# Performance work log

Measured on AMD Instinct MI355X. Metric: run time of the kernel, lower is better.

Reference implementation:

```python
import jax, jax.numpy as jnp
import numpy as np

EXPERT_NUM = 8
SEQ_LEN = 4096
FREQ_LEN = SEQ_LEN // 2 + 1


def setup_inputs() -> dict:
    key = jax.random.key(0)
    ks = jax.random.split(key, 6)
    B, C = 32, 8
    x = jax.random.normal(ks[0], (B, C, SEQ_LEN), dtype=jnp.float32)
    raw = jax.random.uniform(ks[1], (EXPERT_NUM - 1,), dtype=jnp.float32)
    s1 = 1.0 / np.sqrt(FREQ_LEN)
    W1 = jax.random.uniform(ks[2], (FREQ_LEN, FREQ_LEN), jnp.float32, -s1, s1)
    b1 = jax.random.uniform(ks[3], (FREQ_LEN,), jnp.float32, -s1, s1)
    W2 = jax.random.uniform(ks[4], (EXPERT_NUM, FREQ_LEN), jnp.float32, -s1, s1)
    b2 = jax.random.uniform(ks[5], (EXPERT_NUM,), jnp.float32, -s1, s1)
    return {"x": x, "raw": raw, "W1": W1, "b1": b1, "W2": W2, "b2": b2}


def reference(x, raw, W1, b1, W2, b2):
    # instance norm over seq dim (unbiased variance, like torch.var default)
    x_mean = jnp.mean(x, axis=2, keepdims=True)
    xc = x - x_mean
    n = x.shape[2]
    x_var = jnp.sum(xc * xc, axis=2, keepdims=True) / (n - 1) + 1e-5
    xn = xc / jnp.sqrt(x_var)

    freq_x = jnp.fft.rfft(xn, axis=-1)            # [B, C, F] complex
    F_ = freq_x.shape[-1]

    # sorted sigmoid boundaries -> integer band edges (non-differentiable cast)
    b = jnp.sort(jax.nn.sigmoid(raw))
    boundaries = jnp.concatenate([jnp.zeros(1, x.dtype), b, jnp.ones(1, x.dtype)])
    idx = jnp.floor(jax.lax.stop_gradient(boundaries) * F_).astype(jnp.int32)
    idx = idx.at[-1].set(F_)

    # band-pass masks for all experts at once: [E, F]
    fpos = jnp.arange(F_)
    mask = (fpos[None, :] >= idx[:-1, None]) & (fpos[None, :] < idx[1:, None])

    # per-expert frequency components: [B, E, C, F]
    comp = freq_x[:, None, :, :] * mask[None, :, None, :].astype(freq_x.dtype)
    expert_outputs = jnp.fft.irfft(comp, n=SEQ_LEN, axis=-1)  # [B, E, C, L]

    # gating on channel-averaged magnitude spectrum
    gating_input = jnp.mean(jnp.abs(freq_x), axis=1)          # [B, F]
    h = jax.nn.relu(gating_input @ W1.T + b1)
    gating_scores = jax.nn.softmax(h @ W2.T + b2, axis=-1)    # [B, E]

    # gated combine in frequency domain, then single iFFT
    gate_c = gating_scores.astype(freq_x.dtype)
    combined_freq = jnp.einsum('becf,be->bcf', comp, gate_c)
    combined = jnp.fft.irfft(combined_freq, n=SEQ_LEN, axis=-1)
    combined = combined * jnp.sqrt(x_var) + x_mean
    return combined, boundaries, gating_scores, expert_outputs
```

## Files before the change

### kernel.cpp

```cpp
#include <hip/hip_runtime.h>
#include <hip/hip_bf16.h>


using cplx = float2;
typedef float nfloat2 __attribute__((ext_vector_type(2)));

static constexpr int BB = 32, CCH = 8, LL = 4096, FF = 2049, EE = 8;

static constexpr size_t WS_FREQ  = 0;
static constexpr size_t WS_MEAN  = WS_FREQ + (size_t)BB * CCH * FF * 2;
static constexpr size_t WS_SIGMA = WS_MEAN + 256;
static constexpr size_t WS_GI    = WS_SIGMA + 256;
static constexpr size_t WS_H     = WS_GI + (size_t)BB * FF;
static constexpr size_t WS_IDX   = WS_H + (size_t)BB * FF;
static constexpr size_t WS_EOF   = WS_IDX + 16;
static constexpr size_t WS_LOGIT = WS_EOF + 2049;
static constexpr size_t WS_W2048 = WS_LOGIT + 256;
static constexpr size_t WS_U     = WS_W2048 + 4096;

static constexpr size_t OUT_COMB = 0;
static constexpr size_t OUT_BND  = (size_t)BB * CCH * LL;
static constexpr size_t OUT_GATE = OUT_BND + 9;
static constexpr size_t OUT_EXP  = OUT_GATE + (size_t)BB * EE;

#define PHI(i) ((i) + ((i) >> 5))
__device__ __forceinline__ int scat(int n) {
  return ((n & 3) << 9) | (((n >> 2) & 7) << 6) | (((n >> 5) & 7) << 3) | (n >> 8);
}

template <bool INV>
__device__ __forceinline__ void dft8(float* zr, float* zi) {
  const float C = 0.70710678118654752f;
  float s0r = zr[0] + zr[4], s0i = zi[0] + zi[4];
  float d0r = zr[0] - zr[4], d0i = zi[0] - zi[4];
  float s1r = zr[2] + zr[6], s1i = zi[2] + zi[6];
  float d1r = zr[2] - zr[6], d1i = zi[2] - zi[6];
  float E0r = s0r + s1r, E0i = s0i + s1i;
  float E2r = s0r - s1r, E2i = s0i - s1i;
  float E1r, E1i, E3r, E3i;
  if (!INV) { E1r = d0r + d1i; E1i = d0i - d1r; E3r = d0r - d1i; E3i = d0i + d1r; }
  else      { E1r = d0r - d1i; E1i = d0i + d1r; E3r = d0r + d1i; E3i = d0i - d1r; }
  float t0r = zr[1] + zr[5], t0i = zi[1] + zi[5];
  float e0r = zr[1] - zr[5], e0i = zi[1] - zi[5];
  float t1r = zr[3] + zr[7], t1i = zi[3] + zi[7];
  float e1r = zr[3] - zr[7], e1i = zi[3] - zi[7];
  float O0r = t0r + t1r, O0i = t0i + t1i;
  float O2r = t0r - t1r, O2i = t0i - t1i;
  float O1r, O1i, O3r, O3i;
  if (!INV) { O1r = e0r + e1i; O1i = e0i - e1r; O3r = e0r - e1i; O3i = e0i + e1r; }
  else      { O1r = e0r - e1i; O1i = e0i + e1r; O3r = e0r + e1i; O3i = e0i - e1r; }
  float w1r, w1i, w2r, w2i, w3r, w3i;
  if (!INV) {
    w1r = C * (O1r + O1i); w1i = C * (O1i - O1r);
    w2r = O2i;             w2i = -O2r;
    w3r = C * (O3i - O3r); w3i = -C * (O3r + O3i);
  } else {
    w1r = C * (O1r - O1i); w1i = C * (O1i + O1r);
    w2r = -O2i;            w2i = O2r;
    w3r = -C * (O3r + O3i); w3i = C * (O3r - O3i);
  }
  zr[0] = E0r + O0r; zi[0] = E0i + O0i;
  zr[4] = E0r - O0r; zi[4] = E0i - O0i;
  zr[1] = E1r + w1r; zi[1] = E1i + w1i;
  zr[5] = E1r - w1r; zi[5] = E1i - w1i;
  zr[2] = E2r + w2r; zi[2] = E2i + w2i;
  zr[6] = E2r - w2r; zi[6] = E2i - w2i;
  zr[3] = E3r + w3r; zi[3] = E3i + w3i;
  zr[7] = E3r - w3r; zi[7] = E3i - w3i;
}

template <bool INV>
__device__ __forceinline__ void dft4(float* zr, float* zi) {
  float s0r = zr[0] + zr[2], s0i = zi[0] + zi[2];
  float d0r = zr[0] - zr[2], d0i = zi[0] - zi[2];
  float s1r = zr[1] + zr[3], s1i = zi[1] + zi[3];
  float d1r = zr[1] - zr[3], d1i = zi[1] - zi[3];
  zr[0] = s0r + s1r; zi[0] = s0i + s1i;
  zr[2] = s0r - s1r; zi[2] = s0i - s1i;
  if (!INV) { zr[1] = d0r + d1i; zi[1] = d0i - d1r; zr[3] = d0r - d1i; zi[3] = d0i + d1r; }
  else      { zr[1] = d0r - d1i; zi[1] = d0i + d1r; zr[3] = d0r + d1i; zi[3] = d0i - d1r; }
}

template <bool INV>
__device__ void fftr8(float* ZR, float* ZI, const cplx* __restrict__ W, int t) {
  float zr[8], zi[8];
  {
    int base = 8 * t;
#pragma unroll
    for (int m = 0; m < 8; ++m) { int i = PHI(base + m); zr[m] = ZR[i]; zi[m] = ZI[i]; }
    dft8<INV>(zr, zi);
#pragma unroll
    for (int m = 0; m < 8; ++m) { int i = PHI(base + m); ZR[i] = zr[m]; ZI[i] = zi[m]; }
  }
  __syncthreads();
  {
    int g = t & 31, p = t >> 5;
    int base = 64 * g + p;
#pragma unroll
    for (int m = 0; m < 8; ++m) { int i = PHI(base + 8 * m); zr[m] = ZR[i]; zi[m] = ZI[i]; }
#pragma unroll
    for (int m = 1; m < 8; ++m) {
      cplx w = W[32 * m * p];
      float wi = INV ? -w.y : w.y;
      float xr = zr[m] * w.x - zi[m] * wi;
      float xi = zr[m] * wi + zi[m] * w.x;
      zr[m] = xr; zi[m] = xi;
    }
    dft8<INV>(zr, zi);
#pragma unroll
    for (int m = 0; m < 8; ++m) { int i = PHI(base + 8 * m); ZR[i] = zr[m]; ZI[i] = zi[m]; }
  }
  __syncthreads();
  {
    int g = t & 3, p = t >> 2;
    int base = 512 * g + p;
#pragma unroll
    for (int m = 0; m < 8; ++m) { int i = PHI(base + 64 * m); zr[m] = ZR[i]; zi[m] = ZI[i]; }
#pragma unroll
    for (int m = 1; m < 8; ++m) {
      cplx w = W[4 * m * p];
      float wi = INV ? -w.y : w.y;
      float xr = zr[m] * w.x - zi[m] * wi;
      float xi = zr[m] * wi + zi[m] * w.x;
      zr[m] = xr; zi[m] = xi;
    }
    dft8<INV>(zr, zi);
#pragma unroll
    for (int m = 0; m < 8; ++m) { int i = PHI(base + 64 * m); ZR[i] = zr[m]; ZI[i] = zi[m]; }
  }
  __syncthreads();
  {
#pragma unroll
    for (int h = 0; h < 2; ++h) {
      int p = t + (h << 8);
      float yr[4], yi[4];
#pragma unroll
      for (int m = 0; m < 4; ++m) { int i = PHI(p + 512 * m); yr[m] = ZR[i]; yi[m] = ZI[i]; }
#pragma unroll
      for (int m = 1; m < 4; ++m) {
        cplx w = W[m * p];
        float wi = INV ? -w.y : w.y;
        float xr = yr[m] * w.x - yi[m] * wi;
        float xi = yr[m] * wi + yi[m] * w.x;
        yr[m] = xr; yi[m] = xi;
      }
      dft4<INV>(yr, yi);
#pragma unroll
      for (int m = 0; m < 4; ++m) { int i = PHI(p + 512 * m); ZR[i] = yr[m]; ZI[i] = yi[m]; }
    }
  }
  __syncthreads();
}

__global__ void k_misc(const float* __restrict__ raw,
                       float* __restrict__ out,
                       float* __restrict__ ws) {
  const int blk = blockIdx.x, t = threadIdx.x;
  if (blk < 8) {
    int j = blk * 256 + t;
    float sn, cs;
    sincosf(-6.283185307179586f * (float)j / 2048.0f, &sn, &cs);
    ((cplx*)(ws + WS_W2048))[j] = make_float2(cs, sn);
  } else if (blk < 17) {
    int k = (blk - 8) * 256 + t;
    if (k < FF) {
      float sn, cs;
      sincosf(-3.14159265358979323846f * (float)k / 2048.0f, &sn, &cs);
      ((cplx*)(ws + WS_U))[k] = make_float2(cs, sn);
    }
  } else if (blk == 17) {
    __shared__ int idx_s[9];
    if (t == 0) {
      float v[7];
      for (int i = 0; i < 7; ++i) v[i] = 1.0f / (1.0f + expf(-raw[i]));
      for (int a = 1; a < 7; ++a) {
        float key = v[a];
        int q = a - 1;
        while (q >= 0 && v[q] > key) { v[q + 1] = v[q]; --q; }
        v[q + 1] = key;
      }
      float bnd[9];
      bnd[0] = 0.0f; bnd[8] = 1.0f;
      for (int i = 0; i < 7; ++i) bnd[i + 1] = v[i];
      int* wi = (int*)(ws + WS_IDX);
      for (int e = 0; e < 9; ++e) {
        int id = (int)floorf(bnd[e] * (float)FF);
        if (e == 8) id = FF;
        idx_s[e] = id;
        wi[e] = id;
        out[OUT_BND + e] = bnd[e];
      }
    }
    __syncthreads();
    int* eof = (int*)(ws + WS_EOF);
    for (int f = t; f < FF; f += 256) {
      int e = 0;
      for (int q = 1; q < 8; ++q)
        if (f >= idx_s[q]) e = q;
      eof[f] = e;
    }
  } else {
    float4* p = (float4*)(ws + WS_GI);
    const float4 z4 = make_float4(0.f, 0.f, 0.f, 0.f);
    for (int i = (blk - 18) * 256 + t; i < 32784; i += 32 * 256) p[i] = z4;
  }
}

__global__ __launch_bounds__(256) void k_fwd(const float* __restrict__ x,
                                             float* __restrict__ ws) {
  __shared__ float ZR[2112], ZI[2112];
  __shared__ float red[8];
  const int t  = threadIdx.x;
  const int bc = blockIdx.x;
  const int b  = bc >> 3;
  const int lane = t & 63, wid = t >> 6;
  const cplx* W = (const cplx*)(ws + WS_W2048);
  const cplx* U = (const cplx*)(ws + WS_U);
  const float2* xp2 = (const float2*)(x + (size_t)bc * LL);

  float2 v[8];
  float sum = 0.f;
#pragma unroll
  for (int u = 0; u < 8; ++u) {
    v[u] = xp2[t + (u << 8)];
    sum += v[u].x + v[u].y;
  }
#pragma unroll
  for (int off = 32; off > 0; off >>= 1) sum += __shfl_down(sum, off, 64);
  if (lane == 0) red[wid] = sum;
  __syncthreads();
  const float mean = (red[0] + red[1] + red[2] + red[3]) * (1.0f / 4096.0f);

  float ss = 0.f;
#pragma unroll
  for (int u = 0; u < 8; ++u) {
    float dx = v[u].x - mean, dy = v[u].y - mean;
    ss += dx * dx + dy * dy;
  }
#pragma unroll
  for (int off = 32; off > 0; off >>= 1) ss += __shfl_down(ss, off, 64);
  if (lane == 0) red[4 + wid] = ss;
  __syncthreads();
  const float var   = (red[4] + red[5] + red[6] + red[7]) / 4095.0f + 1e-5f;
  const float sigma = sqrtf(var);
  const float inv   = 1.0f / sigma;
  if (t == 0) {
    ws[WS_MEAN + bc]  = mean;
    ws[WS_SIGMA + bc] = sigma;
  }

#pragma unroll
  for (int u = 0; u < 8; ++u) {
    int n = t + (u << 8);
    int i = PHI(scat(n));
    ZR[i] = (v[u].x - mean) * inv;
    ZI[i] = (v[u].y - mean) * inv;
  }
  __syncthreads();

  fftr8<false>(ZR, ZI, W, t);

  cplx* freq = (cplx*)ws + (size_t)bc * FF;
#pragma unroll
  for (int u = 0; u < 9; ++u) {
    int k = t + (u << 8);
    if (k > 2048) break;
    int ka = k & 2047, km = (2048 - k) & 2047;
    float Zkr = ZR[PHI(ka)], Zki = ZI[PHI(ka)];
    float Zmr = ZR[PHI(km)], Zmi = ZI[PHI(km)];
    float fex = 0.5f * (Zkr + Zmr);
    float fey = 0.5f * (Zki - Zmi);
    float fox = 0.5f * (Zki + Zmi);
    float foy = -0.5f * (Zkr - Zmr);
    cplx uk = U[k];
    float rx = fex + uk.x * fox - uk.y * foy;
    float ry = fey + uk.x * foy + uk.y * fox;
    freq[k] = make_float2(rx, ry);
    atomicAdd(&ws[WS_GI + (size_t)b * FF + k], 0.125f * sqrtf(rx * rx + ry * ry));
  }
}

__global__ __launch_bounds__(256) void k_mid(const float* __restrict__ W1,
                                             float* __restrict__ ws,
                                             float* __restrict__ out) {
  __shared__ float SM[4224];
  const int p = blockIdx.x, t = threadIdx.x;

  if (p < 1089) {
    float* W1s = SM;
    float* gis = SM + 2112;
    const int i0 = (p % 33) * 64;
    const int il = t & 63, bg = t >> 6;
    float acc[8] = {0, 0, 0, 0, 0, 0, 0, 0};
    const int fbeg = (p / 33) * 64;
    const int fend = min(fbeg + 64, FF);
    for (int f0 = fbeg; f0 < fend; f0 += 32) {
      for (int q = t; q < 64 * 32; q += 256) {
        int r = q >> 5, cc = q & 31;
        int gi_i = i0 + r, gf = f0 + cc;
        W1s[r * 33 + cc] = (gi_i < FF && gf < FF) ? W1[(size_t)gi_i * FF + gf] : 0.f;
      }
      for (int q = t; q < 32 * 32; q += 256) {
        int bb = q >> 5, cc = q & 31;
        int gf = f0 + cc;
        gis[bb * 33 + cc] = (gf < FF) ? ws[WS_GI + (size_t)bb * FF + gf] : 0.f;
      }
      __syncthreads();
#pragma unroll 8
      for (int cc = 0; cc < 32; ++cc) {
        float wv = W1s[il * 33 + cc];
#pragma unroll
        for (int j = 0; j < 8; ++j) acc[j] += wv * gis[(bg * 8 + j) * 33 + cc];
      }
      __syncthreads();
    }
    int ii = i0 + il;
    if (ii < FF) {
#pragma unroll
      for (int j = 0; j < 8; ++j)
        atomicAdd(&ws[WS_H + (size_t)(bg * 8 + j) * FF + ii], acc[j]);
    }
    return;
  }
  if (p < 1096) return;

  const int e9  = p - 1096;
  const int xcd = e9 & 7, slot = e9 >> 3;
  const int bc  = ((slot >> 3) << 3) | xcd;
  const int j   = slot & 7;
  const int b   = bc >> 3, c = bc & 7;

  float* ZR = SM;
  float* ZI = SM + 2112;
  const cplx* freq = (const cplx*)ws + (size_t)bc * FF;
  const int*  idxp = (const int*)(ws + WS_IDX);
  const cplx* W    = (const cplx*)(ws + WS_W2048);
  const cplx* U    = (const cplx*)(ws + WS_U);
  const int lo = idxp[j], hi = idxp[j + 1];

#pragma unroll
  for (int u = 0; u < 8; ++u) {
    int k  = t + (u << 8);
    int km = 2048 - k;
    cplx A = make_float2(0.f, 0.f), Bv = make_float2(0.f, 0.f);
    if (k >= lo && k < hi)   A  = freq[k];
    if (km >= lo && km < hi) Bv = freq[km];
    float Px = A.x - Bv.x, Py = A.y + Bv.y;
    float Qx = A.x + Bv.x, Qy = A.y - Bv.y;
    cplx uk = U[k];
    float cs = uk.x, sn = -uk.y;
    float Xox = 0.5f * (cs * Px - sn * Py);
    float Xoy = 0.5f * (cs * Py + sn * Px);
    int i = PHI(scat(k));
    ZR[i] = 0.5f * Qx - Xoy;
    ZI[i] = 0.5f * Qy + Xox;
  }
  __syncthreads();

  fftr8<true>(ZR, ZI, W, t);

  const float mul = 1.0f / 2048.0f;
  float* op = out + OUT_EXP + (((size_t)(b * EE + j) * CCH + c) * LL);
  if (t == 0) __builtin_nontemporal_store(ZR[PHI(0)] * mul, op);
#pragma unroll
  for (int u = 0; u < 8; ++u) {
    int n = t + (u << 8);
    if (n < 2047) {
      nfloat2 o;
      o.x = ZI[PHI(n)] * mul;
      o.y = ZR[PHI(n + 1)] * mul;
      __builtin_nontemporal_store(o, (nfloat2*)(op + 2 * n + 1));
    } else {
      __builtin_nontemporal_store(ZI[PHI(2047)] * mul, op + 4095);
    }
  }
}

__global__ __launch_bounds__(256) void k_comb(const float* __restrict__ b1,
                                              const float* __restrict__ W2,
                                              const float* __restrict__ b2,
                                              const float* __restrict__ ws,
                                              float* __restrict__ out) {
  __shared__ float ZR[2112], ZI[2112];
  __shared__ float red[4][8];
  __shared__ float lg[8];
  __shared__ float gates_s[8];
  const int t  = threadIdx.x;
  const int bc = blockIdx.x;
  const int b  = bc >> 3, c = bc & 7;
  const int lane = t & 63, wid = t >> 6;

  float pacc[8] = {0, 0, 0, 0, 0, 0, 0, 0};
  const float* hrow = ws + WS_H + (size_t)b * FF;
  for (int f = t; f < FF; f += 256) {
    float hv = fmaxf(hrow[f] + b1[f], 0.f);
#pragma unroll
    for (int e = 0; e < 8; ++e) pacc[e] += hv * W2[(size_t)e * FF + f];
  }
#pragma unroll
  for (int off = 32; off > 0; off >>= 1) {
#pragma unroll
    for (int e = 0; e < 8; ++e) pacc[e] += __shfl_down(pacc[e], off, 64);
  }
  if (lane == 0) {
#pragma unroll
    for (int e = 0; e < 8; ++e) red[wid][e] = pacc[e];
  }
  __syncthreads();
  if (t < 8) lg[t] = red[0][t] + red[1][t] + red[2][t] + red[3][t] + b2[t];
  __syncthreads();
  if (t < 8) {
    float mx = lg[0];
#pragma unroll
    for (int q = 1; q < 8; ++q) mx = fmaxf(mx, lg[q]);
    float sm = 0.f;
#pragma unroll
    for (int q = 0; q < 8; ++q) sm += expf(lg[q] - mx);
    float g = expf(lg[t] - mx) / sm;
    gates_s[t] = g;
    if (c == 0) out[OUT_GATE + (size_t)b * 8 + t] = g;
  }
  __syncthreads();

  const cplx* freq = (const cplx*)ws + (size_t)bc * FF;
  const int*  eof  = (const int*)(ws + WS_EOF);
  const cplx* W    = (const cplx*)(ws + WS_W2048);
  const cplx* U    = (const cplx*)(ws + WS_U);

#pragma unroll
  for (int u = 0; u < 8; ++u) {
    int k  = t + (u << 8);
    int km = 2048 - k;
    cplx A  = freq[k];
    cplx Bv = freq[km];
    float gk = gates_s[eof[k]], gm = gates_s[eof[km]];
    A.x *= gk; A.y *= gk; Bv.x *= gm; Bv.y *= gm;
    float Px = A.x - Bv.x, Py = A.y + Bv.y;
    float Qx = A.x + Bv.x, Qy = A.y - Bv.y;
    cplx uk = U[k];
    float cs = uk.x, sn = -uk.y;
    float Xox = 0.5f * (cs * Px - sn * Py);
    float Xoy = 0.5f * (cs * Py + sn * Px);
    int i = PHI(scat(k));
    ZR[i] = 0.5f * Qx - Xoy;
    ZI[i] = 0.5f * Qy + Xox;
  }
  __syncthreads();

  fftr8<true>(ZR, ZI, W, t);

  const float mul = ws[WS_SIGMA + bc] * (1.0f / 2048.0f);
  const float add = ws[WS_MEAN + bc];
  nfloat2* op = (nfloat2*)(out + OUT_COMB + (size_t)bc * LL);
#pragma unroll
  for (int u = 0; u < 8; ++u) {
    int n = t + (u << 8);
    nfloat2 o;
    o.x = ZR[PHI(n)] * mul + add;
    o.y = ZI[PHI(n)] * mul + add;
    __builtin_nontemporal_store(o, op + n);
  }
}

extern "C" void kernel_launch(void* const* d_in, const int* in_sizes, int n_in,
                              void* d_out, int out_size, void* d_ws, size_t ws_size,
                              hipStream_t stream) {
  const float* x   = (const float*)d_in[0];
  const float* raw = (const float*)d_in[1];
  const float* W1  = (const float*)d_in[2];
  const float* b1  = (const float*)d_in[3];
  const float* W2  = (const float*)d_in[4];
  const float* b2  = (const float*)d_in[5];
  float* out = (float*)d_out;
  float* ws  = (float*)d_ws;

  k_misc<<<50, 256, 0, stream>>>(raw, out, ws);
  k_fwd<<<BB * CCH, 256, 0, stream>>>(x, ws);
  k_mid<<<1096 + 2048, 256, 0, stream>>>(W1, ws, out);
  k_comb<<<BB * CCH, 256, 0, stream>>>(b1, W2, b2, ws, out);
}
```

Measured before the change: 134.8 us.

## Fold misc kernel into forward FFT and rebalance expert iFFTs across kernels

```diff
diff --git a/kernel.cpp b/kernel.cpp
--- a/kernel.cpp
+++ b/kernel.cpp
@@ -10,18 +10,19 @@
 static constexpr size_t WS_FREQ  = 0;
 static constexpr size_t WS_MEAN  = WS_FREQ + (size_t)BB * CCH * FF * 2;
 static constexpr size_t WS_SIGMA = WS_MEAN + 256;
-static constexpr size_t WS_GI    = WS_SIGMA + 256;
-static constexpr size_t WS_H     = WS_GI + (size_t)BB * FF;
+static constexpr size_t WS_AMAG  = WS_SIGMA + 256;
+static constexpr size_t WS_H     = WS_AMAG + (size_t)BB * CCH * FF;
 static constexpr size_t WS_IDX   = WS_H + (size_t)BB * FF;
 static constexpr size_t WS_EOF   = WS_IDX + 16;
-static constexpr size_t WS_LOGIT = WS_EOF + 2049;
-static constexpr size_t WS_W2048 = WS_LOGIT + 256;
-static constexpr size_t WS_U     = WS_W2048 + 4096;
 
 static constexpr size_t OUT_COMB = 0;
 static constexpr size_t OUT_BND  = (size_t)BB * CCH * LL;
 static constexpr size_t OUT_GATE = OUT_BND + 9;
 static constexpr size_t OUT_EXP  = OUT_GATE + (size_t)BB * EE;
+
+__device__ float2 g_W2048[2048];
+__device__ float2 g_U[2049];
+__device__ int    g_tabcnt = 0;
 
 #define PHI(i) ((i) + ((i) >> 5))
 __device__ __forceinline__ int scat(int n) {
@@ -152,70 +153,124 @@
   __syncthreads();
 }
 
-__global__ void k_misc(const float* __restrict__ raw,
-                       float* __restrict__ out,
-                       float* __restrict__ ws) {
-  const int blk = blockIdx.x, t = threadIdx.x;
-  if (blk < 8) {
-    int j = blk * 256 + t;
-    float sn, cs;
-    sincosf(-6.283185307179586f * (float)j / 2048.0f, &sn, &cs);
-    ((cplx*)(ws + WS_W2048))[j] = make_float2(cs, sn);
-  } else if (blk < 17) {
-    int k = (blk - 8) * 256 + t;
-    if (k < FF) {
-      float sn, cs;
-      sincosf(-3.14159265358979323846f * (float)k / 2048.0f, &sn, &cs);
-      ((cplx*)(ws + WS_U))[k] = make_float2(cs, sn);
-    }
-  } else if (blk == 17) {
-    __shared__ int idx_s[9];
-    if (t == 0) {
-      float v[7];
-      for (int i = 0; i < 7; ++i) v[i] = 1.0f / (1.0f + expf(-raw[i]));
-      for (int a = 1; a < 7; ++a) {
-        float key = v[a];
-        int q = a - 1;
-        while (q >= 0 && v[q] > key) { v[q + 1] = v[q]; --q; }
-        v[q + 1] = key;
-      }
-      float bnd[9];
-      bnd[0] = 0.0f; bnd[8] = 1.0f;
-      for (int i = 0; i < 7; ++i) bnd[i + 1] = v[i];
-      int* wi = (int*)(ws + WS_IDX);
-      for (int e = 0; e < 9; ++e) {
-        int id = (int)floorf(bnd[e] * (float)FF);
-        if (e == 8) id = FF;
-        idx_s[e] = id;
-        wi[e] = id;
-        out[OUT_BND + e] = bnd[e];
-      }
-    }
-    __syncthreads();
-    int* eof = (int*)(ws + WS_EOF);
-    for (int f = t; f < FF; f += 256) {
-      int e = 0;
-      for (int q = 1; q < 8; ++q)
-        if (f >= idx_s[q]) e = q;
-      eof[f] = e;
-    }
-  } else {
-    float4* p = (float4*)(ws + WS_GI);
-    const float4 z4 = make_float4(0.f, 0.f, 0.f, 0.f);
-    for (int i = (blk - 18) * 256 + t; i < 32784; i += 32 * 256) p[i] = z4;
+__device__ __forceinline__ void expert_ifft(const float* __restrict__ ws,
+                                            float* __restrict__ out,
+                                            float* ZR, float* ZI,
+                                            int bc, int j, int t) {
+  const int b = bc >> 3, c = bc & 7;
+  const cplx* freq = (const cplx*)ws + (size_t)bc * FF;
+  const int*  idxp = (const int*)(ws + WS_IDX);
+  const int lo = idxp[j], hi = idxp[j + 1];
+
+#pragma unroll
+  for (int u = 0; u < 8; ++u) {
+    int k  = t + (u << 8);
+    int km = 2048 - k;
+    cplx A = make_float2(0.f, 0.f), Bv = make_float2(0.f, 0.f);
+    if (k >= lo && k < hi)   A  = freq[k];
+    if (km >= lo && km < hi) Bv = freq[km];
+    float Px = A.x - Bv.x, Py = A.y + Bv.y;
+    float Qx = A.x + Bv.x, Qy = A.y - Bv.y;
+    cplx uk = g_U[k];
+    float cs = uk.x, sn = -uk.y;
+    float Xox = 0.5f * (cs * Px - sn * Py);
+    float Xoy = 0.5f * (cs * Py + sn * Px);
+    int i = PHI(scat(k));
+    ZR[i] = 0.5f * Qx - Xoy;
+    ZI[i] = 0.5f * Qy + Xox;
+  }
+  __syncthreads();
+
+  fftr8<true>(ZR, ZI, g_W2048, t);
+
+  const float mul = 1.0f / 2048.0f;
+  float* op = out + OUT_EXP + (((size_t)(b * EE + j) * CCH + c) * LL);
+  if (t == 0) __builtin_nontemporal_store(ZR[PHI(0)] * mul, op);
+#pragma unroll
+  for (int u = 0; u < 8; ++u) {
+    int n = t + (u << 8);
+    if (n < 2047) {
+      nfloat2 o;
+      o.x = ZI[PHI(n)] * mul;
+      o.y = ZR[PHI(n + 1)] * mul;
+      __builtin_nontemporal_store(o, (nfloat2*)(op + 2 * n + 1));
+    } else {
+      __builtin_nontemporal_store(ZI[PHI(2047)] * mul, op + 4095);
+    }
   }
 }
 
 __global__ __launch_bounds__(256) void k_fwd(const float* __restrict__ x,
-                                             float* __restrict__ ws) {
+                                             const float* __restrict__ raw,
+                                             float* __restrict__ ws,
+                                             float* __restrict__ out) {
+  const int p = blockIdx.x, t = threadIdx.x;
+
+  if (p >= 256) {
+    if (p < 273) {
+      if (__hip_atomic_load(&g_tabcnt, __ATOMIC_RELAXED, __HIP_MEMORY_SCOPE_AGENT) < 17) {
+        if (p < 264) {
+          int jj = (p - 256) * 256 + t;
+          float sn, cs;
+          sincosf(-6.283185307179586f * (float)jj / 2048.0f, &sn, &cs);
+          g_W2048[jj] = make_float2(cs, sn);
+        } else {
+          int k = (p - 264) * 256 + t;
+          if (k < FF) {
+            float sn, cs;
+            sincosf(-3.14159265358979323846f * (float)k / 2048.0f, &sn, &cs);
+            g_U[k] = make_float2(cs, sn);
+          }
+        }
+        __syncthreads();
+        if (t == 0) {
+          __threadfence();
+          __hip_atomic_fetch_add(&g_tabcnt, 1, __ATOMIC_RELEASE, __HIP_MEMORY_SCOPE_AGENT);
+        }
+      }
+    } else if (p == 273) {
+      __shared__ int idx_s[9];
+      if (t == 0) {
+        float v[7];
+        for (int i = 0; i < 7; ++i) v[i] = 1.0f / (1.0f + expf(-raw[i]));
+        for (int a = 1; a < 7; ++a) {
+          float key = v[a];
+          int q = a - 1;
+          while (q >= 0 && v[q] > key) { v[q + 1] = v[q]; --q; }
+          v[q + 1] = key;
+        }
+        float bnd[9];
+        bnd[0] = 0.0f; bnd[8] = 1.0f;
+        for (int i = 0; i < 7; ++i) bnd[i + 1] = v[i];
+        int* wi = (int*)(ws + WS_IDX);
+        for (int e = 0; e < 9; ++e) {
+          int id = (int)floorf(bnd[e] * (float)FF);
+          if (e == 8) id = FF;
+          idx_s[e] = id;
+          wi[e] = id;
+          out[OUT_BND + e] = bnd[e];
+        }
+      }
+      __syncthreads();
+      int* eof = (int*)(ws + WS_EOF);
+      for (int f = t; f < FF; f += 256) {
+        int e = 0;
+        for (int q = 1; q < 8; ++q)
+          if (f >= idx_s[q]) e = q;
+        eof[f] = e;
+      }
+    } else {
+      float4* hp = (float4*)(ws + WS_H);
+      const float4 z4 = make_float4(0.f, 0.f, 0.f, 0.f);
+      for (int i = (p - 274) * 256 + t; i < 16392; i += 8 * 256) hp[i] = z4;
+    }
+    return;
+  }
+
   __shared__ float ZR[2112], ZI[2112];
   __shared__ float red[8];
-  const int t  = threadIdx.x;
-  const int bc = blockIdx.x;
-  const int b  = bc >> 3;
+  const int bc = p;
   const int lane = t & 63, wid = t >> 6;
-  const cplx* W = (const cplx*)(ws + WS_W2048);
-  const cplx* U = (const cplx*)(ws + WS_U);
   const float2* xp2 = (const float2*)(x + (size_t)bc * LL);
 
   float2 v[8];
@@ -256,9 +311,14 @@
     ZR[i] = (v[u].x - mean) * inv;
     ZI[i] = (v[u].y - mean) * inv;
   }
-  __syncthreads();
-
-  fftr8<false>(ZR, ZI, W, t);
+  if (t == 0) {
+    while (__hip_atomic_load(&g_tabcnt, __ATOMIC_ACQUIRE, __HIP_MEMORY_SCOPE_AGENT) < 17) {
+      __builtin_amdgcn_s_sleep(8);
+    }
+  }
+  __syncthreads();
+
+  fftr8<false>(ZR, ZI, g_W2048, t);
 
   cplx* freq = (cplx*)ws + (size_t)bc * FF;
 #pragma unroll
@@ -272,11 +332,11 @@
     float fey = 0.5f * (Zki - Zmi);
     float fox = 0.5f * (Zki + Zmi);
     float foy = -0.5f * (Zkr - Zmr);
-    cplx uk = U[k];
+    cplx uk = g_U[k];
     float rx = fex + uk.x * fox - uk.y * foy;
     float ry = fey + uk.x * foy + uk.y * fox;
     freq[k] = make_float2(rx, ry);
-    atomicAdd(&ws[WS_GI + (size_t)b * FF + k], 0.125f * sqrtf(rx * rx + ry * ry));
+    ws[WS_AMAG + (size_t)bc * FF + k] = 0.125f * sqrtf(rx * rx + ry * ry);
   }
 }
 
@@ -303,7 +363,13 @@
       for (int q = t; q < 32 * 32; q += 256) {
         int bb = q >> 5, cc = q & 31;
         int gf = f0 + cc;
-        gis[bb * 33 + cc] = (gf < FF) ? ws[WS_GI + (size_t)bb * FF + gf] : 0.f;
+        float s = 0.f;
+        if (gf < FF) {
+          const float* ap = ws + WS_AMAG + (size_t)(bb * 8) * FF + gf;
+#pragma unroll
+          for (int c = 0; c < 8; ++c) s += ap[(size_t)c * FF];
+        }
+        gis[bb * 33 + cc] = s;
       }
       __syncthreads();
 #pragma unroll 8
@@ -324,56 +390,12 @@
   }
   if (p < 1096) return;
 
-  const int e9  = p - 1096;
-  const int xcd = e9 & 7, slot = e9 >> 3;
-  const int bc  = ((slot >> 3) << 3) | xcd;
-  const int j   = slot & 7;
-  const int b   = bc >> 3, c = bc & 7;
-
-  float* ZR = SM;
-  float* ZI = SM + 2112;
-  const cplx* freq = (const cplx*)ws + (size_t)bc * FF;
-  const int*  idxp = (const int*)(ws + WS_IDX);
-  const cplx* W    = (const cplx*)(ws + WS_W2048);
-  const cplx* U    = (const cplx*)(ws + WS_U);
-  const int lo = idxp[j], hi = idxp[j + 1];
-
-#pragma unroll
-  for (int u = 0; u < 8; ++u) {
-    int k  = t + (u << 8);
-    int km = 2048 - k;
-    cplx A = make_float2(0.f, 0.f), Bv = make_float2(0.f, 0.f);
-    if (k >= lo && k < hi)   A  = freq[k];
-    if (km >= lo && km < hi) Bv = freq[km];
-    float Px = A.x - Bv.x, Py = A.y + Bv.y;
-    float Qx = A.x + Bv.x, Qy = A.y - Bv.y;
-    cplx uk = U[k];
-    float cs = uk.x, sn = -uk.y;
-    float Xox = 0.5f * (cs * Px - sn * Py);
-    float Xoy = 0.5f * (cs * Py + sn * Px);
-    int i = PHI(scat(k));
-    ZR[i] = 0.5f * Qx - Xoy;
-    ZI[i] = 0.5f * Qy + Xox;
-  }
-  __syncthreads();
-
-  fftr8<true>(ZR, ZI, W, t);
-
-  const float mul = 1.0f / 2048.0f;
-  float* op = out + OUT_EXP + (((size_t)(b * EE + j) * CCH + c) * LL);
-  if (t == 0) __builtin_nontemporal_store(ZR[PHI(0)] * mul, op);
-#pragma unroll
-  for (int u = 0; u < 8; ++u) {
-    int n = t + (u << 8);
-    if (n < 2047) {
-      nfloat2 o;
-      o.x = ZI[PHI(n)] * mul;
-      o.y = ZR[PHI(n + 1)] * mul;
-      __builtin_nontemporal_store(o, (nfloat2*)(op + 2 * n + 1));
-    } else {
-      __builtin_nontemporal_store(ZI[PHI(2047)] * mul, op + 4095);
-    }
-  }
+  const int e   = p - 1096;
+  const int xcd = e & 7, s = e >> 3;
+  const int grp = s / 6, j = s % 6;
+  const int bc  = (grp << 3) | xcd;
+
+  expert_ifft(ws, out, SM, SM + 2112, bc, j, t);
 }
 
 __global__ __launch_bounds__(256) void k_comb(const float* __restrict__ b1,
@@ -382,11 +404,19 @@
                                               const float* __restrict__ ws,
                                               float* __restrict__ out) {
   __shared__ float ZR[2112], ZI[2112];
+  const int p = blockIdx.x, t = threadIdx.x;
+
+  if (p >= 256) {
+    const int q  = p - 256;
+    const int jj = q >> 8, bc = q & 255;
+    expert_ifft(ws, out, ZR, ZI, bc, 6 + jj, t);
+    return;
+  }
+
   __shared__ float red[4][8];
   __shared__ float lg[8];
   __shared__ float gates_s[8];
-  const int t  = threadIdx.x;
-  const int bc = blockIdx.x;
+  const int bc = p;
   const int b  = bc >> 3, c = bc & 7;
   const int lane = t & 63, wid = t >> 6;
 
@@ -424,8 +454,6 @@
 
   const cplx* freq = (const cplx*)ws + (size_t)bc * FF;
   const int*  eof  = (const int*)(ws + WS_EOF);
-  const cplx* W    = (const cplx*)(ws + WS_W2048);
-  const cplx* U    = (const cplx*)(ws + WS_U);
 
 #pragma unroll
   for (int u = 0; u < 8; ++u) {
@@ -437,7 +465,7 @@
     A.x *= gk; A.y *= gk; Bv.x *= gm; Bv.y *= gm;
     float Px = A.x - Bv.x, Py = A.y + Bv.y;
     float Qx = A.x + Bv.x, Qy = A.y - Bv.y;
-    cplx uk = U[k];
+    cplx uk = g_U[k];
     float cs = uk.x, sn = -uk.y;
     float Xox = 0.5f * (cs * Px - sn * Py);
     float Xoy = 0.5f * (cs * Py + sn * Px);
@@ -447,7 +475,7 @@
   }
   __syncthreads();
 
-  fftr8<true>(ZR, ZI, W, t);
+  fftr8<true>(ZR, ZI, g_W2048, t);
 
   const float mul = ws[WS_SIGMA + bc] * (1.0f / 2048.0f);
   const float add = ws[WS_MEAN + bc];
@@ -474,8 +502,7 @@
   float* out = (float*)d_out;
   float* ws  = (float*)d_ws;
 
-  k_misc<<<50, 256, 0, stream>>>(raw, out, ws);
-  k_fwd<<<BB * CCH, 256, 0, stream>>>(x, ws);
-  k_mid<<<1096 + 2048, 256, 0, stream>>>(W1, ws, out);
-  k_comb<<<BB * CCH, 256, 0, stream>>>(b1, W2, b2, ws, out);
-}
+  k_fwd<<<282, 256, 0, stream>>>(x, raw, ws, out);
+  k_mid<<<1096 + 1536, 256, 0, stream>>>(W1, ws, out);
+  k_comb<<<256 + 512, 256, 0, stream>>>(b1, W2, b2, ws, out);
+}
```

Measured after the change: 135.1 us. No clear change (+0.2%).
